# Kernel tuning notes

Hardware: AMD Instinct MI355X
Metric: run time of the kernel (lower is better)

The kernel has to match this reference:

```python
import math
import jax, jax.numpy as jnp
import numpy as np

H_HEADS = 8
SR = 2


def _layernorm(x, w, b, eps=1e-5):
    mu = jnp.mean(x, axis=-1, keepdims=True)
    var = jnp.mean((x - mu) ** 2, axis=-1, keepdims=True)
    return (x - mu) / jnp.sqrt(var + eps) * w + b


def _dwconv(x, w, b, pad, stride=1):
    # x: (B,C,H,W), w: (C,1,kh,kw) depthwise
    y = jax.lax.conv_general_dilated(
        x, w, (stride, stride), padding=pad,
        dimension_numbers=('NCHW', 'OIHW', 'NCHW'),
        feature_group_count=x.shape[1])
    return y + b[None, :, None, None]


def _lpu(x, w3, b3, w51, b51, w15, b15):
    # LocalPerceptionUint (act=False): x + dw3x3(x) + dw1x5(dw5x1(x))
    out = _dwconv(x, w3, b3, [(1, 1), (1, 1)])
    out2 = _dwconv(_dwconv(x, w51, b51, [(2, 2), (0, 0)]), w15, b15, [(0, 0), (2, 2)])
    return x + out + out2


def _split_halves(x, B, C, N, h, w):
    # faithful to torch: permute(0,2,1).reshape(B,C,N//2,2) then per-slice permute+reshape
    x_ = x.transpose(0, 2, 1).reshape(B, C, N // 2, 2)
    x1 = x_[..., 0].transpose(0, 2, 1).reshape(B, C, h, w)
    x2 = x_[..., 1].transpose(0, 2, 1).reshape(B, C, h, w)
    return x1, x2


def reference(x, ln_in_w, ln_in_b, ln_out_w, ln_out_b,
              lpu1_w3, lpu1_b3, lpu1_w51, lpu1_b51, lpu1_w15, lpu1_b15,
              lpu2_w3, lpu2_b3, lpu2_w51, lpu2_b51, lpu2_w15, lpu2_b15,
              q_w, q_b, kv_w, kv_b, proj_w, proj_b,
              sr1_w, sr1_b, sr2_w, sr2_b, sa_norm_w, sa_norm_b,
              mlp_w1, mlp_b1, mlp_w2, mlp_b2):
    B, N, C = x.shape
    h = int(math.isqrt(N // 2)); w = h
    dh = C // H_HEADS

    # ---- LPU on two interleaved halves ----
    x1, x2 = _split_halves(x, B, C, N, h, w)
    x1 = x1 + _lpu(x1, lpu1_w3, lpu1_b3, lpu1_w51, lpu1_b51, lpu1_w15, lpu1_b15)
    x2 = x2 + _lpu(x2, lpu2_w3, lpu2_b3, lpu2_w51, lpu2_b51, lpu2_w15, lpu2_b15)
    x = jnp.concatenate([x1, x2], axis=2).reshape(B, C, -1).transpose(0, 2, 1)  # (B,N,C)

    # ---- SelfAttention on LayerNorm(x) ----
    xa = _layernorm(x, ln_in_w, ln_in_b)
    q = (xa @ q_w.T + q_b).reshape(B, N, H_HEADS, dh).transpose(0, 2, 1, 3)  # (B,H,N,dh)

    xs1, xs2 = _split_halves(xa, B, C, N, h, w)
    xcat = jnp.concatenate([xs1, xs2], axis=2)  # (B,C,2h,w)
    pad = SR // 2
    xshift = jnp.pad(xcat, ((0, 0), (0, 0), (pad, 0), (pad, 0)))  # top/left pad
    y1 = _dwconv(xcat, sr1_w, sr1_b, [(0, 0), (0, 0)], stride=SR)
    y2 = _dwconv(xshift, sr2_w, sr2_b, [(0, 0), (0, 0)], stride=SR)
    Hs, Ws = y1.shape[2], y1.shape[3]
    y2 = y2[:, :, :Hs, :Ws]
    xk = jnp.stack([y1.reshape(B, C, -1), y2.reshape(B, C, -1)], axis=3)
    xk = xk.reshape(B, C, -1).transpose(0, 2, 1)  # (B, Nk, C), interleaved
    xk = _layernorm(xk, sa_norm_w, sa_norm_b)
    kv = (xk @ kv_w.T + kv_b).reshape(B, -1, 2, H_HEADS, dh).transpose(2, 0, 3, 1, 4)
    k, v = kv[0], kv[1]  # (B,H,Nk,dh)

    attn = jnp.einsum('bhnd,bhmd->bhnm', q, k) * (dh ** -0.5)
    M = attn.shape[-1]
    if 101 < M < 10000:  # static shape -> Python branch, matches torch gate
        topk = int(M * 0.8)
        idx = jax.lax.top_k(attn, topk)[1]  # (B,H,N,topk)
        bi = jnp.arange(B)[:, None, None, None]
        hi = jnp.arange(H_HEADS)[None, :, None, None]
        ni = jnp.arange(N)[None, None, :, None]
        mask = jnp.zeros(attn.shape, dtype=bool).at[bi, hi, ni, idx].set(True)
        attn = jnp.where(mask, attn, -jnp.inf)
    attn = jax.nn.softmax(attn, axis=-1)
    sa = jnp.einsum('bhnm,bhmd->bhnd', attn, v).transpose(0, 2, 1, 3).reshape(B, N, C)
    sa = sa @ proj_w.T + proj_b

    x = x + sa
    xm = _layernorm(x, ln_out_w, ln_out_b)
    hid = jax.nn.gelu(xm @ mlp_w1.T + mlp_b1, approximate=False)
    x = x + (hid @ mlp_w2.T + mlp_b2)
    return x


def setup_inputs():
    C = 512
    E = 4
    ks = iter(jax.random.split(jax.random.key(0), 24))

    def w(shape, std=0.02):
        return jax.random.normal(next(ks), shape, jnp.float32) * std

    inp = {"x": jax.random.normal(next(ks), (4, 2048, C), jnp.float32)}
    for nm in ("ln_in", "ln_out", "sa_norm"):
        inp[nm + "_w"] = jnp.ones((C,), jnp.float32)
        inp[nm + "_b"] = jnp.zeros((C,), jnp.float32)
    for p in ("lpu1", "lpu2"):
        inp[p + "_w3"] = w((C, 1, 3, 3))
        inp[p + "_b3"] = jnp.zeros((C,), jnp.float32)
        inp[p + "_w51"] = w((C, 1, 5, 1))
        inp[p + "_b51"] = jnp.zeros((C,), jnp.float32)
        inp[p + "_w15"] = w((C, 1, 1, 5))
        inp[p + "_b15"] = jnp.zeros((C,), jnp.float32)
    inp["q_w"] = w((C, C)); inp["q_b"] = jnp.zeros((C,), jnp.float32)
    inp["kv_w"] = w((2 * C, C)); inp["kv_b"] = jnp.zeros((2 * C,), jnp.float32)
    inp["proj_w"] = w((C, C)); inp["proj_b"] = jnp.zeros((C,), jnp.float32)
    inp["sr1_w"] = w((C, 1, SR, SR)); inp["sr1_b"] = jnp.zeros((C,), jnp.float32)
    inp["sr2_w"] = w((C, 1, SR, SR)); inp["sr2_b"] = jnp.zeros((C,), jnp.float32)
    inp["mlp_w1"] = w((E * C, C)); inp["mlp_b1"] = jnp.zeros((E * C,), jnp.float32)
    inp["mlp_w2"] = w((C, E * C)); inp["mlp_b2"] = jnp.zeros((C,), jnp.float32)
    return inp
```

## Files before the change

kernel.cpp:

```cpp
#include <hip/hip_runtime.h>
#include <stdint.h>

#define DEVI __device__ __forceinline__
typedef unsigned short u16;
typedef __attribute__((ext_vector_type(8))) short bf8v;
typedef __attribute__((ext_vector_type(4))) float f4v;

DEVI u16 f2bf(float f) {
  union { float f; uint32_t u; } v; v.f = f;
  return (u16)((v.u + 0x7fffu + ((v.u >> 16) & 1u)) >> 16);
}
DEVI float bf2f(u16 b) {
  union { uint32_t u; float f; } v; v.u = ((uint32_t)b) << 16;
  return v.f;
}
DEVI f4v mfma16(bf8v a, bf8v b, f4v c) {
  return __builtin_amdgcn_mfma_f32_16x16x32_bf16(a, b, c, 0, 0, 0);
}
DEVI void gload16(const u16* g, u16* l) {
  const auto* gp = reinterpret_cast<const uint32_t __attribute__((address_space(1)))*>(
      reinterpret_cast<uintptr_t>(g));
  auto* lp = reinterpret_cast<uint32_t __attribute__((address_space(3)))*>(
      reinterpret_cast<uintptr_t>(l));
  __builtin_amdgcn_global_load_lds(gp, lp, 16, 0, 0);
}

__global__ void cvt_kernel(const float4* __restrict__ s, ushort4* __restrict__ d, int n4) {
  int i = blockIdx.x * 256 + threadIdx.x;
  if (i < n4) {
    float4 v = s[i];
    ushort4 o; o.x = f2bf(v.x); o.y = f2bf(v.y); o.z = f2bf(v.z); o.w = f2bf(v.w);
    d[i] = o;
  }
}

__global__ __launch_bounds__(256) void lpu_kernel(
    const float* __restrict__ x, float* __restrict__ xp,
    const float* __restrict__ w3a, const float* __restrict__ b3a,
    const float* __restrict__ w51a, const float* __restrict__ b51a,
    const float* __restrict__ w15a, const float* __restrict__ b15a,
    const float* __restrict__ w3b, const float* __restrict__ b3b,
    const float* __restrict__ w51b, const float* __restrict__ b51b,
    const float* __restrict__ w15b, const float* __restrict__ b15b)
{
  __shared__ float xt[36 * 36];
  __shared__ float yt[32 * 36];
  int bid = blockIdx.x;
  int cp = bid & 511, img = (bid >> 9) & 1, b = bid >> 10;
  const float* W3  = (img ? w3b  : w3a)  + cp * 9;
  const float* W51 = (img ? w51b : w51a) + cp * 5;
  const float* W15 = (img ? w15b : w15a) + cp * 5;
  float B3  = (img ? b3b  : b3a)[cp];
  float B51 = (img ? b51b : b51a)[cp];
  float B15 = (img ? b15b : b15a)[cp];
  int t = threadIdx.x;
  for (int i = t; i < 36 * 36; i += 256) xt[i] = 0.f;
  for (int i = t; i < 32 * 36; i += 256) yt[i] = 0.f;
  __syncthreads();
  {
    int s = t * 4;
    int row = 4 * cp + 2 * (s >> 9) + img;
    float4 v = *(const float4*)(x + ((size_t)b * 2048 + row) * 512 + (s & 511));
    float* dp = &xt[(2 + (s >> 5)) * 36 + 2 + (s & 31)];
    dp[0] = v.x; dp[1] = v.y; dp[2] = v.z; dp[3] = v.w;
  }
  __syncthreads();
  float w3r[9], w51r[5], w15r[5];
  #pragma unroll
  for (int i = 0; i < 9; i++) w3r[i] = W3[i];
  #pragma unroll
  for (int i = 0; i < 5; i++) { w51r[i] = W51[i]; w15r[i] = W15[i]; }
  #pragma unroll
  for (int pp = 0; pp < 4; pp++) {
    int s = t + pp * 256;
    int i = s >> 5, j = s & 31;
    float a = B51;
    #pragma unroll
    for (int di = 0; di < 5; di++) a += w51r[di] * xt[(i + di) * 36 + 2 + j];
    yt[i * 36 + 2 + j] = a;
  }
  __syncthreads();
  #pragma unroll
  for (int pp = 0; pp < 4; pp++) {
    int s = t + pp * 256;
    int i = s >> 5, j = s & 31;
    float o = 2.f * xt[(2 + i) * 36 + 2 + j] + B3 + B15;
    #pragma unroll
    for (int di = 0; di < 3; di++)
      #pragma unroll
      for (int dj = 0; dj < 3; dj++)
        o += w3r[di * 3 + dj] * xt[(1 + i + di) * 36 + 1 + j + dj];
    #pragma unroll
    for (int dj = 0; dj < 5; dj++) o += w15r[dj] * yt[i * 36 + j + dj];
    xp[((size_t)b * 2048 + img * 1024 + s) * 512 + cp] = o;
  }
}

template<int WF32, int WBF>
__global__ __launch_bounds__(256) void ln_kernel(
    const float* __restrict__ x, const float* __restrict__ w, const float* __restrict__ bb,
    float* __restrict__ of, u16* __restrict__ ob)
{
  int row = blockIdx.x * 4 + (threadIdx.x >> 6);
  int lane = threadIdx.x & 63;
  const float4* xr = (const float4*)(x + (size_t)row * 512);
  float4 v0 = xr[lane], v1 = xr[64 + lane];
  float s = v0.x + v0.y + v0.z + v0.w + v1.x + v1.y + v1.z + v1.w;
  #pragma unroll
  for (int off = 32; off; off >>= 1) s += __shfl_xor(s, off);
  float mu = s * (1.f / 512.f);
  float q = 0.f, d;
  d = v0.x - mu; q += d * d;  d = v0.y - mu; q += d * d;
  d = v0.z - mu; q += d * d;  d = v0.w - mu; q += d * d;
  d = v1.x - mu; q += d * d;  d = v1.y - mu; q += d * d;
  d = v1.z - mu; q += d * d;  d = v1.w - mu; q += d * d;
  #pragma unroll
  for (int off = 32; off; off >>= 1) q += __shfl_xor(q, off);
  float rstd = rsqrtf(q * (1.f / 512.f) + 1e-5f);
  const float4* w4 = (const float4*)w;
  const float4* b4 = (const float4*)bb;
  float4 wa = w4[lane], wc = w4[64 + lane], ba = b4[lane], bc = b4[64 + lane];
  float4 y0, y1;
  y0.x = (v0.x - mu) * rstd * wa.x + ba.x;  y0.y = (v0.y - mu) * rstd * wa.y + ba.y;
  y0.z = (v0.z - mu) * rstd * wa.z + ba.z;  y0.w = (v0.w - mu) * rstd * wa.w + ba.w;
  y1.x = (v1.x - mu) * rstd * wc.x + bc.x;  y1.y = (v1.y - mu) * rstd * wc.y + bc.y;
  y1.z = (v1.z - mu) * rstd * wc.z + bc.z;  y1.w = (v1.w - mu) * rstd * wc.w + bc.w;
  if (WF32) {
    float4* o = (float4*)(of + (size_t)row * 512);
    o[lane] = y0; o[64 + lane] = y1;
  }
  if (WBF) {
    ushort4 p0, p1;
    p0.x = f2bf(y0.x); p0.y = f2bf(y0.y); p0.z = f2bf(y0.z); p0.w = f2bf(y0.w);
    p1.x = f2bf(y1.x); p1.y = f2bf(y1.y); p1.z = f2bf(y1.z); p1.w = f2bf(y1.w);
    ushort4* o = (ushort4*)(ob + (size_t)row * 512);
    o[lane] = p0; o[64 + lane] = p1;
  }
}

__global__ __launch_bounds__(256) void sr_kernel(
    const float* __restrict__ xa,
    const float* __restrict__ w1, const float* __restrict__ b1,
    const float* __restrict__ w2, const float* __restrict__ b2,
    float* __restrict__ xk)
{
  __shared__ float img[2048];
  int bid = blockIdx.x;
  int c = bid & 511, b = bid >> 9;
  int t = threadIdx.x;
  {
    int idx = t * 4;
    #pragma unroll
    for (int p = 0; p < 2; p++) {
      int ii = idx + p * 1024;
      int k = ii >> 9, off = ii & 511;
      int perm = (k == 1) ? 2 : ((k == 2) ? 1 : k);
      float4 v = *(const float4*)(xa + ((size_t)b * 2048 + 4 * c + perm) * 512 + off);
      *(float4*)&img[ii] = v;
    }
  }
  __syncthreads();
  float W1[4], W2[4];
  #pragma unroll
  for (int i = 0; i < 4; i++) { W1[i] = w1[c * 4 + i]; W2[i] = w2[c * 4 + i]; }
  float B1 = b1[c], B2 = b2[c];
  #pragma unroll
  for (int pp = 0; pp < 2; pp++) {
    int s = t + pp * 256;
    int p = s >> 4, q = s & 15;
    int u = 2 * p, v = 2 * q;
    float y1 = B1 + W1[0] * img[u * 32 + v]       + W1[1] * img[u * 32 + v + 1]
                  + W1[2] * img[(u + 1) * 32 + v] + W1[3] * img[(u + 1) * 32 + v + 1];
    float y2 = B2;
    #pragma unroll
    for (int di = 0; di < 2; di++)
      #pragma unroll
      for (int dj = 0; dj < 2; dj++) {
        int uu = u + di - 1, vv = v + dj - 1;
        float xv = (uu >= 0 && vv >= 0) ? img[uu * 32 + vv] : 0.f;
        y2 += W2[di * 2 + dj] * xv;
      }
    size_t base = ((size_t)b * 1024 + 2 * s) * 512 + c;
    xk[base] = y1;
    xk[base + 512] = y2;
  }
}

template<int EPI>
__global__ __launch_bounds__(256) void gemm_bt(
    const u16* __restrict__ A, const u16* __restrict__ W, const float* __restrict__ bias,
    void* __restrict__ out, const float* __restrict__ res, void* __restrict__ out2,
    int M, int N, int K)
{
  __shared__ u16 As[128 * 32];
  __shared__ u16 Bs[128 * 32];
  int tid = threadIdx.x;
  int wid = tid >> 6, lane = tid & 63;
  int wr = wid >> 1, wc = wid & 1;
  int l15 = lane & 15, lhi = lane >> 4;
  int m0 = blockIdx.y * 128, n0 = blockIdx.x * 128;
  f4v acc[4][4] = {};
  int srow = lane >> 2;
  int scol = (lane & 3) * 8;
  const u16* ap0 = &A[(size_t)(m0 + wid * 32 + srow) * K + scol];
  const u16* ap1 = &A[(size_t)(m0 + wid * 32 + 16 + srow) * K + scol];
  const u16* bp0 = &W[(size_t)(n0 + wid * 32 + srow) * K + scol];
  const u16* bp1 = &W[(size_t)(n0 + wid * 32 + 16 + srow) * K + scol];
  u16* al0 = &As[(wid * 32) * 32];
  u16* al1 = &As[(wid * 32 + 16) * 32];
  u16* bl0 = &Bs[(wid * 32) * 32];
  u16* bl1 = &Bs[(wid * 32 + 16) * 32];
  for (int k0 = 0; k0 < K; k0 += 32) {
    gload16(ap0 + k0, al0);
    gload16(ap1 + k0, al1);
    gload16(bp0 + k0, bl0);
    gload16(bp1 + k0, bl1);
    __syncthreads();
    bf8v af[4], bfr[4];
    #pragma unroll
    for (int mi = 0; mi < 4; mi++) af[mi] = *(const bf8v*)&As[(wr * 64 + mi * 16 + l15) * 32 + lhi * 8];
    #pragma unroll
    for (int ni = 0; ni < 4; ni++) bfr[ni] = *(const bf8v*)&Bs[(wc * 64 + ni * 16 + l15) * 32 + lhi * 8];
    #pragma unroll
    for (int mi = 0; mi < 4; mi++)
      #pragma unroll
      for (int ni = 0; ni < 4; ni++)
        acc[mi][ni] = mfma16(af[mi], bfr[ni], acc[mi][ni]);
    __syncthreads();
  }
  #pragma unroll
  for (int mi = 0; mi < 4; mi++) {
    #pragma unroll
    for (int ni = 0; ni < 4; ni++) {
      int col = n0 + wc * 64 + ni * 16 + l15;
      float bv = bias[col];
      #pragma unroll
      for (int r = 0; r < 4; r++) {
        int row = m0 + wr * 64 + mi * 16 + lhi * 4 + r;
        float v = acc[mi][ni][r] + bv;
        if (EPI == 0) {
          int b = row >> 11, n = row & 2047, h = col >> 6, dd = col & 63;
          ((u16*)out)[(((size_t)(b * 8 + h) * 2048) + n) * 64 + dd] = f2bf(v);
        } else if (EPI == 1) {
          int b = row >> 10, m = row & 1023;
          if (col < 512) {
            int h = col >> 6, dd = col & 63;
            ((u16*)out)[(((size_t)(b * 8 + h) * 1024) + m) * 64 + dd] = f2bf(v);
          } else {
            int h = (col - 512) >> 6, dd = col & 63;
            ((u16*)out2)[(((size_t)(b * 8 + h) * 64) + dd) * 1024 + m] = f2bf(v);
          }
        } else if (EPI == 2) {
          size_t idx = (size_t)row * N + col;
          ((float*)out)[idx] = v + res[idx];
        } else {
          float g = 0.5f * v * (1.f + erff(v * 0.70710678118f));
          ((u16*)out)[(size_t)row * N + col] = f2bf(g);
        }
      }
    }
  }
}

__global__ __launch_bounds__(256, 4) void attn_kernel(
    const u16* __restrict__ qg, const u16* __restrict__ kg,
    const u16* __restrict__ vTg, u16* __restrict__ sa)
{
  __shared__ u16 S16[16 * 1024];
  __shared__ float thr[16], mx[16], dn[16];
  int bid = blockIdx.x;
  int qt = bid & 127, bh = bid >> 7;
  int q0 = qt * 16;
  int tid = threadIdx.x, w = tid >> 6, lane = tid & 63;
  int l15 = lane & 15, lhi = lane >> 4;
  const u16* qbase = qg + ((size_t)bh * 2048 + q0) * 64;
  bf8v aq0 = *(const bf8v*)&qbase[l15 * 64 + lhi * 8];
  bf8v aq1 = *(const bf8v*)&qbase[l15 * 64 + 32 + lhi * 8];
  const u16* kbase = kg + (size_t)bh * 1024 * 64;
  for (int ct = 0; ct < 16; ct++) {
    int kc0 = w * 256 + ct * 16;
    const u16* kb = &kbase[(size_t)(kc0 + l15) * 64 + lhi * 8];
    bf8v bk0 = *(const bf8v*)&kb[0];
    bf8v bk1 = *(const bf8v*)&kb[32];
    f4v a = {};
    a = mfma16(aq0, bk0, a);
    a = mfma16(aq1, bk1, a);
    #pragma unroll
    for (int r = 0; r < 4; r++) {
      int row = lhi * 4 + r;
      int col = kc0 + l15;
      S16[row * 1024 + (col ^ ((row & 7) << 3))] = f2bf(a[r] * 0.125f);
    }
  }
  __syncthreads();
  for (int rr = 0; rr < 4; rr++) {
    int row = w * 4 + rr;
    int pat = (row & 7) << 3;
    float vals[16];
    #pragma unroll
    for (int j = 0; j < 16; j++) vals[j] = bf2f(S16[row * 1024 + ((j * 64 + lane) ^ pat)]);
    float vmax = vals[0], vmin = vals[0];
    #pragma unroll
    for (int j = 1; j < 16; j++) { vmax = fmaxf(vmax, vals[j]); vmin = fminf(vmin, vals[j]); }
    #pragma unroll
    for (int off = 32; off; off >>= 1) {
      vmax = fmaxf(vmax, __shfl_xor(vmax, off));
      vmin = fminf(vmin, __shfl_xor(vmin, off));
    }
    float lo = vmin, hi = vmax;
    for (int it = 0; it < 14; it++) {
      float mid = 0.5f * (lo + hi);
      int cnt = 0;
      #pragma unroll
      for (int j = 0; j < 16; j++) cnt += (int)__popcll(__ballot(vals[j] >= mid));
      if (cnt >= 819) lo = mid; else hi = mid;
    }
    if (lane == 0) { thr[row] = lo; mx[row] = vmax; }
  }
  __syncthreads();
  {
    int row = tid >> 4, cg = tid & 15;
    int pat = (row & 7) << 3;
    float m = mx[row], T = thr[row];
    float ls = 0.f;
    for (int j = 0; j < 64; j++) {
      int idx = row * 1024 + ((cg + j * 16) ^ pat);
      float sv = bf2f(S16[idx]);
      float pv = (sv >= T) ? __expf(sv - m) : 0.f;
      S16[idx] = f2bf(pv);
      ls += pv;
    }
    #pragma unroll
    for (int off = 8; off; off >>= 1) ls += __shfl_xor(ls, off);
    if (cg == 0) dn[row] = ls;
  }
  __syncthreads();
  f4v oacc = {};
  const u16* vb = vTg + ((size_t)bh * 64 + w * 16 + l15) * 1024;
  int patp = (l15 & 7) << 3;
  for (int ks = 0; ks < 32; ks++) {
    int m0 = ks * 32;
    bf8v ap = *(const bf8v*)&S16[l15 * 1024 + ((m0 + lhi * 8) ^ patp)];
    bf8v bv = *(const bf8v*)&vb[m0 + lhi * 8];
    oacc = mfma16(ap, bv, oacc);
  }
  int b = bh >> 3, h = bh & 7;
  #pragma unroll
  for (int r = 0; r < 4; r++) {
    int row = lhi * 4 + r;
    float ov = oacc[r] / dn[row];
    sa[((size_t)b * 2048 + q0 + row) * 512 + h * 64 + w * 16 + l15] = f2bf(ov);
  }
}

extern "C" void kernel_launch(void* const* d_in, const int* in_sizes, int n_in,
                              void* d_out, int out_size, void* d_ws, size_t ws_size,
                              hipStream_t stream) {
  (void)in_sizes; (void)n_in; (void)out_size; (void)ws_size;
  const float* x        = (const float*)d_in[0];
  const float* ln_in_w  = (const float*)d_in[1];
  const float* ln_in_b  = (const float*)d_in[2];
  const float* ln_out_w = (const float*)d_in[3];
  const float* ln_out_b = (const float*)d_in[4];
  const float* sa_w     = (const float*)d_in[5];
  const float* sa_b     = (const float*)d_in[6];
  const float* q_w      = (const float*)d_in[19];
  const float* q_b      = (const float*)d_in[20];
  const float* kv_w     = (const float*)d_in[21];
  const float* kv_b     = (const float*)d_in[22];
  const float* proj_w   = (const float*)d_in[23];
  const float* proj_b   = (const float*)d_in[24];
  const float* sr1_w    = (const float*)d_in[25];
  const float* sr1_b    = (const float*)d_in[26];
  const float* sr2_w    = (const float*)d_in[27];
  const float* sr2_b    = (const float*)d_in[28];
  const float* mlp_w1   = (const float*)d_in[29];
  const float* mlp_b1   = (const float*)d_in[30];
  const float* mlp_w2   = (const float*)d_in[31];
  const float* mlp_b2   = (const float*)d_in[32];

  uint8_t* ws = (uint8_t*)d_ws;
  float* xp   = (float*)(ws + 0);
  float* xa   = (float*)(ws + 16777216);
  u16*  hid   = (u16*)(ws + 0);
  u16*  xab   = (u16*)(ws + 33554432);
  u16*  qb    = (u16*)(ws + 41943040);
  float* xk   = (float*)(ws + 50331648);
  u16*  xkb   = (u16*)(ws + 58720256);
  u16*  kb    = (u16*)(ws + 62914560);
  u16*  vTb   = (u16*)(ws + 67108864);
  u16*  sab   = (u16*)(ws + 71303168);
  float* x2   = (float*)(ws + 79691776);
  u16*  xmb   = (u16*)(ws + 96468992);
  u16*  wqb   = (u16*)(ws + 104857600);
  u16*  wkvb  = (u16*)(ws + 105381888);
  u16*  wprojb= (u16*)(ws + 106430464);
  u16*  wm1b  = (u16*)(ws + 106954752);
  u16*  wm2b  = (u16*)(ws + 109051904);

  auto cvt = [&](const float* s, u16* d, int n) {
    int n4 = n / 4;
    cvt_kernel<<<dim3((n4 + 255) / 256), dim3(256), 0, stream>>>((const float4*)s, (ushort4*)d, n4);
  };
  cvt(q_w, wqb, 512 * 512);
  cvt(kv_w, wkvb, 1024 * 512);
  cvt(proj_w, wprojb, 512 * 512);
  cvt(mlp_w1, wm1b, 2048 * 512);
  cvt(mlp_w2, wm2b, 512 * 2048);

  lpu_kernel<<<dim3(4096), dim3(256), 0, stream>>>(
      x, xp,
      (const float*)d_in[7],  (const float*)d_in[8],  (const float*)d_in[9],
      (const float*)d_in[10], (const float*)d_in[11], (const float*)d_in[12],
      (const float*)d_in[13], (const float*)d_in[14], (const float*)d_in[15],
      (const float*)d_in[16], (const float*)d_in[17], (const float*)d_in[18]);

  ln_kernel<1, 1><<<dim3(2048), dim3(256), 0, stream>>>(xp, ln_in_w, ln_in_b, xa, xab);

  sr_kernel<<<dim3(2048), dim3(256), 0, stream>>>(xa, sr1_w, sr1_b, sr2_w, sr2_b, xk);

  ln_kernel<0, 1><<<dim3(1024), dim3(256), 0, stream>>>(xk, sa_w, sa_b, nullptr, xkb);

  gemm_bt<0><<<dim3(4, 64), dim3(256), 0, stream>>>(xab, wqb, q_b, (void*)qb, nullptr, nullptr, 8192, 512, 512);
  gemm_bt<1><<<dim3(8, 32), dim3(256), 0, stream>>>(xkb, wkvb, kv_b, (void*)kb, nullptr, (void*)vTb, 4096, 1024, 512);

  attn_kernel<<<dim3(4096), dim3(256), 0, stream>>>(qb, kb, vTb, sab);

  gemm_bt<2><<<dim3(4, 64), dim3(256), 0, stream>>>(sab, wprojb, proj_b, (void*)x2, xp, nullptr, 8192, 512, 512);

  ln_kernel<0, 1><<<dim3(2048), dim3(256), 0, stream>>>(x2, ln_out_w, ln_out_b, nullptr, xmb);

  gemm_bt<3><<<dim3(16, 64), dim3(256), 0, stream>>>(xmb, wm1b, mlp_b1, (void*)hid, nullptr, nullptr, 8192, 2048, 512);
  gemm_bt<2><<<dim3(4, 64), dim3(256), 0, stream>>>(hid, wm2b, mlp_b2, d_out, x2, nullptr, 8192, 512, 2048);
}
```

Measured before the change: 515.9 us.

## Halve GEMM M-tile to 64 rows and fuse softmax exp into threshold pass

The GEMM block tile drops from 128x128 to 64x128, with each warp covering 32 rows and the launch grids doubled. This raises the block count for the small 8192x512 GEMMs so more CUs are filled, at the cost of reloading more weight tiles per output. In attention, the exponentiation and row-sum are now done from the register values already held by the top-k threshold search. This removes a syncthreads, a second shared-memory read pass, and the thr/mx shared arrays.

```diff
diff --git a/kernel.cpp b/kernel.cpp
--- a/kernel.cpp
+++ b/kernel.cpp
@@ -192,51 +192,47 @@
     void* __restrict__ out, const float* __restrict__ res, void* __restrict__ out2,
     int M, int N, int K)
 {
-  __shared__ u16 As[128 * 32];
+  __shared__ u16 As[64 * 32];
   __shared__ u16 Bs[128 * 32];
   int tid = threadIdx.x;
   int wid = tid >> 6, lane = tid & 63;
   int wr = wid >> 1, wc = wid & 1;
   int l15 = lane & 15, lhi = lane >> 4;
-  int m0 = blockIdx.y * 128, n0 = blockIdx.x * 128;
-  f4v acc[4][4] = {};
-  int srow = lane >> 2;
-  int scol = (lane & 3) * 8;
-  const u16* ap0 = &A[(size_t)(m0 + wid * 32 + srow) * K + scol];
-  const u16* ap1 = &A[(size_t)(m0 + wid * 32 + 16 + srow) * K + scol];
-  const u16* bp0 = &W[(size_t)(n0 + wid * 32 + srow) * K + scol];
-  const u16* bp1 = &W[(size_t)(n0 + wid * 32 + 16 + srow) * K + scol];
-  u16* al0 = &As[(wid * 32) * 32];
-  u16* al1 = &As[(wid * 32 + 16) * 32];
-  u16* bl0 = &Bs[(wid * 32) * 32];
-  u16* bl1 = &Bs[(wid * 32 + 16) * 32];
+  int m0 = blockIdx.y * 64, n0 = blockIdx.x * 128;
+  f4v acc[2][4] = {};
+  int trow = tid >> 2, tcol = (tid & 3) * 8;
+  const u16* apg  = &A[(size_t)(m0 + trow) * K + tcol];
+  const u16* bpg0 = &W[(size_t)(n0 + trow) * K + tcol];
+  const u16* bpg1 = &W[(size_t)(n0 + 64 + trow) * K + tcol];
+  u16* al  = &As[tid * 8];
+  u16* bl0 = &Bs[tid * 8];
+  u16* bl1 = &Bs[2048 + tid * 8];
   for (int k0 = 0; k0 < K; k0 += 32) {
-    gload16(ap0 + k0, al0);
-    gload16(ap1 + k0, al1);
-    gload16(bp0 + k0, bl0);
-    gload16(bp1 + k0, bl1);
+    gload16(apg + k0, al);
+    gload16(bpg0 + k0, bl0);
+    gload16(bpg1 + k0, bl1);
     __syncthreads();
-    bf8v af[4], bfr[4];
-    #pragma unroll
-    for (int mi = 0; mi < 4; mi++) af[mi] = *(const bf8v*)&As[(wr * 64 + mi * 16 + l15) * 32 + lhi * 8];
+    bf8v af[2], bfr[4];
+    #pragma unroll
+    for (int mi = 0; mi < 2; mi++) af[mi] = *(const bf8v*)&As[(wr * 32 + mi * 16 + l15) * 32 + lhi * 8];
     #pragma unroll
     for (int ni = 0; ni < 4; ni++) bfr[ni] = *(const bf8v*)&Bs[(wc * 64 + ni * 16 + l15) * 32 + lhi * 8];
     #pragma unroll
-    for (int mi = 0; mi < 4; mi++)
+    for (int mi = 0; mi < 2; mi++)
       #pragma unroll
       for (int ni = 0; ni < 4; ni++)
         acc[mi][ni] = mfma16(af[mi], bfr[ni], acc[mi][ni]);
     __syncthreads();
   }
   #pragma unroll
-  for (int mi = 0; mi < 4; mi++) {
+  for (int mi = 0; mi < 2; mi++) {
     #pragma unroll
     for (int ni = 0; ni < 4; ni++) {
       int col = n0 + wc * 64 + ni * 16 + l15;
       float bv = bias[col];
       #pragma unroll
       for (int r = 0; r < 4; r++) {
-        int row = m0 + wr * 64 + mi * 16 + lhi * 4 + r;
+        int row = m0 + wr * 32 + mi * 16 + lhi * 4 + r;
         float v = acc[mi][ni][r] + bv;
         if (EPI == 0) {
           int b = row >> 11, n = row & 2047, h = col >> 6, dd = col & 63;
@@ -267,7 +263,7 @@
     const u16* __restrict__ vTg, u16* __restrict__ sa)
 {
   __shared__ u16 S16[16 * 1024];
-  __shared__ float thr[16], mx[16], dn[16];
+  __shared__ float dn[16];
   int bid = blockIdx.x;
   int qt = bid & 127, bh = bid >> 7;
   int q0 = qt * 16;
@@ -315,24 +311,16 @@
       for (int j = 0; j < 16; j++) cnt += (int)__popcll(__ballot(vals[j] >= mid));
       if (cnt >= 819) lo = mid; else hi = mid;
     }
-    if (lane == 0) { thr[row] = lo; mx[row] = vmax; }
-  }
-  __syncthreads();
-  {
-    int row = tid >> 4, cg = tid & 15;
-    int pat = (row & 7) << 3;
-    float m = mx[row], T = thr[row];
     float ls = 0.f;
-    for (int j = 0; j < 64; j++) {
-      int idx = row * 1024 + ((cg + j * 16) ^ pat);
-      float sv = bf2f(S16[idx]);
-      float pv = (sv >= T) ? __expf(sv - m) : 0.f;
-      S16[idx] = f2bf(pv);
+    #pragma unroll
+    for (int j = 0; j < 16; j++) {
+      float pv = (vals[j] >= lo) ? __expf(vals[j] - vmax) : 0.f;
       ls += pv;
-    }
-    #pragma unroll
-    for (int off = 8; off; off >>= 1) ls += __shfl_xor(ls, off);
-    if (cg == 0) dn[row] = ls;
+      S16[row * 1024 + ((j * 64 + lane) ^ pat)] = f2bf(pv);
+    }
+    #pragma unroll
+    for (int off = 32; off; off >>= 1) ls += __shfl_xor(ls, off);
+    if (lane == 0) dn[row] = ls;
   }
   __syncthreads();
   f4v oacc = {};
@@ -421,15 +409,15 @@
 
   ln_kernel<0, 1><<<dim3(1024), dim3(256), 0, stream>>>(xk, sa_w, sa_b, nullptr, xkb);
 
-  gemm_bt<0><<<dim3(4, 64), dim3(256), 0, stream>>>(xab, wqb, q_b, (void*)qb, nullptr, nullptr, 8192, 512, 512);
-  gemm_bt<1><<<dim3(8, 32), dim3(256), 0, stream>>>(xkb, wkvb, kv_b, (void*)kb, nullptr, (void*)vTb, 4096, 1024, 512);
+  gemm_bt<0><<<dim3(4, 128), dim3(256), 0, stream>>>(xab, wqb, q_b, (void*)qb, nullptr, nullptr, 8192, 512, 512);
+  gemm_bt<1><<<dim3(8, 64), dim3(256), 0, stream>>>(xkb, wkvb, kv_b, (void*)kb, nullptr, (void*)vTb, 4096, 1024, 512);
 
   attn_kernel<<<dim3(4096), dim3(256), 0, stream>>>(qb, kb, vTb, sab);
 
-  gemm_bt<2><<<dim3(4, 64), dim3(256), 0, stream>>>(sab, wprojb, proj_b, (void*)x2, xp, nullptr, 8192, 512, 512);
+  gemm_bt<2><<<dim3(4, 128), dim3(256), 0, stream>>>(sab, wprojb, proj_b, (void*)x2, xp, nullptr, 8192, 512, 512);
 
   ln_kernel<0, 1><<<dim3(2048), dim3(256), 0, stream>>>(x2, ln_out_w, ln_out_b, nullptr, xmb);
 
-  gemm_bt<3><<<dim3(16, 64), dim3(256), 0, stream>>>(xmb, wm1b, mlp_b1, (void*)hid, nullptr, nullptr, 8192, 2048, 512);
-  gemm_bt<2><<<dim3(4, 64), dim3(256), 0, stream>>>(hid, wm2b, mlp_b2, d_out, x2, nullptr, 8192, 512, 2048);
-}
+  gemm_bt<3><<<dim3(16, 128), dim3(256), 0, stream>>>(xmb, wm1b, mlp_b1, (void*)hid, nullptr, nullptr, 8192, 2048, 512);
+  gemm_bt<2><<<dim3(4, 128), dim3(256), 0, stream>>>(hid, wm2b, mlp_b2, d_out, x2, nullptr, 8192, 512, 2048);
+}
```

Result: faster. 486.1 us (-5.8%).
